# Performance work log

Hardware: AMD Instinct MI355X
Metric: run time of the kernel (lower is better)

Reference implementation:

```python
import jax, jax.numpy as jnp
import numpy as np

N_NODES = 50000
N_EDGES = 800000
NODE_DIM = 128
EDGE_DIM = 10
IN_DIM = 2 * NODE_DIM + EDGE_DIM
BN_EPS = 1e-5


def setup_inputs() -> dict:
    key = jax.random.key(0)
    ks = jax.random.split(key, 8)
    h = jax.random.normal(ks[0], (N_NODES, NODE_DIM), dtype=jnp.float32)
    edge_index = jax.random.randint(ks[1], (2, N_EDGES), 0, N_NODES, dtype=jnp.int64)
    edge_feat = jax.random.normal(ks[2], (N_EDGES, EDGE_DIM), dtype=jnp.float32)
    scale = 1.0 / np.sqrt(IN_DIM)
    gate_w = jax.random.normal(ks[3], (IN_DIM, NODE_DIM), dtype=jnp.float32) * scale
    gate_b = jax.random.normal(ks[4], (NODE_DIM,), dtype=jnp.float32) * scale
    cand_w = jax.random.normal(ks[5], (IN_DIM, NODE_DIM), dtype=jnp.float32) * scale
    cand_b = jax.random.normal(ks[6], (NODE_DIM,), dtype=jnp.float32) * scale
    bn_gamma = jnp.ones((NODE_DIM,), dtype=jnp.float32)
    bn_beta = jnp.zeros((NODE_DIM,), dtype=jnp.float32)
    return {"h": h, "edge_index": edge_index, "edge_feat": edge_feat,
            "gate_w": gate_w, "gate_b": gate_b, "cand_w": cand_w, "cand_b": cand_b,
            "bn_gamma": bn_gamma, "bn_beta": bn_beta}


def reference(h, edge_index, edge_feat, gate_w, gate_b, cand_w, cand_b, bn_gamma, bn_beta):
    src = edge_index[0]
    dst = edge_index[1]
    # gather endpoint features and concat with edge features: [E, 2*D + De]
    z = jnp.concatenate([h[src], h[dst], edge_feat], axis=1)
    g = jax.nn.sigmoid(z @ gate_w + gate_b)   # [E, D]
    c = jax.nn.softplus(z @ cand_w + cand_b)  # [E, D]
    m = g * c
    # scatter-add messages to source nodes (matches index_add_(0, src, m))
    agg = jax.ops.segment_sum(m, src, num_segments=h.shape[0])
    # BatchNorm1d in training mode: batch mean / biased variance over nodes
    mean = jnp.mean(agg, axis=0)
    var = jnp.var(agg, axis=0)
    agg_bn = (agg - mean) * jax.lax.rsqrt(var + BN_EPS) * bn_gamma + bn_beta
    return jax.nn.softplus(h + agg_bn)
```

## Files before the change

### kernel.cpp

```cpp
#include <hip/hip_runtime.h>
#include <math.h>

#define N_NODES 50000
#define N_EDGES 800000
#define D 128
#define DE 10
#define K_TOT 266
#define TE 64
#define N_TILES (N_EDGES / TE)
#define ZSTRIDE 296
#define MSTRIDE 129
#define WP_ELEMS (9 * 16 * 64 * 8)
#define SCAN_BLOCKS 196
#define CSTRIDE 16

typedef __bf16 bf16x8 __attribute__((ext_vector_type(8)));
typedef __bf16 bf16x4 __attribute__((ext_vector_type(4)));
typedef __bf16 bf16x2 __attribute__((ext_vector_type(2)));
typedef float  f32x4  __attribute__((ext_vector_type(4)));

__device__ __forceinline__ float fast_sigmoid(float x) {
    float t = __builtin_amdgcn_exp2f(-1.44269504089f * x);
    return __builtin_amdgcn_rcpf(1.0f + t);
}
__device__ __forceinline__ float fast_softplus(float x) {
    float t = __builtin_amdgcn_exp2f(-1.44269504089f * fabsf(x));
    return fmaxf(x, 0.0f) + 0.69314718056f * __builtin_amdgcn_logf(1.0f + t);
}

__global__ __launch_bounds__(256) void prep(
    const float* __restrict__ h, const float* __restrict__ gw,
    const float* __restrict__ cw, const int* __restrict__ ei,
    __bf16* __restrict__ hb, __bf16* __restrict__ wp,
    int* __restrict__ counts)
{
    int bx = blockIdx.x, t = threadIdx.x;
    if (bx < 6250) {
        int i4 = bx * 256 + t;
        float4 v = *(const float4*)&h[(size_t)i4 * 4];
        bf16x4 o = { (__bf16)v.x, (__bf16)v.y, (__bf16)v.z, (__bf16)v.w };
        *(bf16x4*)&hb[(size_t)i4 * 4] = o;
    } else if (bx < 6538) {
        int idx = (bx - 6250) * 256 + t;
        if (idx < WP_ELEMS) {
            int j    = idx & 7;
            int lane = (idx >> 3) & 63;
            int nb   = (idx >> 9) & 15;
            int kb   = idx >> 13;
            int k    = kb * 32 + ((lane >> 4) << 3) + j;
            int col  = ((nb >> 1) << 4) + (lane & 15);
            const float* w = (nb & 1) ? cw : gw;
            float v = (k < K_TOT) ? w[k * D + col] : 0.0f;
            wp[idx] = (__bf16)v;
        }
    } else {
        int e = (bx - 6538) * 256 + t;
        atomicAdd(&counts[ei[e] * CSTRIDE], 1);
    }
}

__global__ __launch_bounds__(256) void scan_partials(
    const int* __restrict__ counts, int* __restrict__ bsum)
{
    __shared__ int ss[256];
    int t = threadIdx.x;
    int i = blockIdx.x * 256 + t;
    int c = (i < N_NODES) ? counts[i * CSTRIDE] : 0;
    ss[t] = c;
    __syncthreads();
    #pragma unroll
    for (int off = 1; off < 256; off <<= 1) {
        int v = (t >= off) ? ss[t - off] : 0;
        __syncthreads();
        ss[t] += v;
        __syncthreads();
    }
    if (t == 255) bsum[blockIdx.x] = ss[255];
}

__global__ __launch_bounds__(256) void scan_final(
    int* __restrict__ counts, const int* __restrict__ bsum)
{
    __shared__ int sb[256];
    __shared__ int ss[256];
    int t = threadIdx.x;
    sb[t] = (t < SCAN_BLOCKS) ? bsum[t] : 0;
    int i = blockIdx.x * 256 + t;
    int c = (i < N_NODES) ? counts[i * CSTRIDE] : 0;
    ss[t] = c;
    __syncthreads();
    #pragma unroll
    for (int off = 1; off < 256; off <<= 1) {
        int v  = (t >= off) ? ss[t - off] : 0;
        int vb = (t >= off) ? sb[t - off] : 0;
        __syncthreads();
        ss[t] += v;
        sb[t] += vb;
        __syncthreads();
    }
    int base = blockIdx.x ? sb[blockIdx.x - 1] : 0;
    if (i < N_NODES) counts[i * CSTRIDE] = base + ss[t] - c;
}

__global__ __launch_bounds__(256) void csr_scatter(
    const int* __restrict__ ei, int* __restrict__ cursor,
    int2* __restrict__ sdp, int* __restrict__ eidx)
{
    int e = blockIdx.x * 256 + threadIdx.x;
    int node = ei[e];
    int pos = atomicAdd(&cursor[node * CSTRIDE], 1);
    sdp[pos] = make_int2(node, ei[N_EDGES + e]);
    eidx[pos] = e;
}

__global__ __launch_bounds__(256, 4) void edge_mfma_scatter(
    const __bf16* __restrict__ hb, const int2* __restrict__ sdp,
    const float* __restrict__ ef, const __bf16* __restrict__ wp,
    const float* __restrict__ gb, const float* __restrict__ cb,
    const int* __restrict__ eidx, float* __restrict__ agg)
{
    __shared__ __align__(16) unsigned char smem[TE * ZSTRIDE * 2];
    __shared__ int s_eid[TE], s_src[TE], s_dst[TE];
    __bf16* zs = (__bf16*)smem;
    float*  ms = (float*)smem;

    const int t  = threadIdx.x;
    const int e0 = blockIdx.x * TE;

    if (t < TE) {
        int2 p = sdp[e0 + t];
        s_src[t] = p.x;
        s_dst[t] = p.y;
        s_eid[t] = eidx[e0 + t];
    }
    __syncthreads();

    #pragma unroll
    for (int it = 0; it < 8; ++it) {
        int lin = it * 256 + t;
        int region = lin >> 10;
        int r   = (lin >> 4) & 63;
        int seg = lin & 15;
        int node = region ? s_dst[r] : s_src[r];
        bf16x8 v = *(const bf16x8*)&hb[(size_t)node * D + seg * 8];
        *(bf16x8*)&zs[r * ZSTRIDE + region * 128 + seg * 8] = v;
    }
    if (t < TE) {
        const float* efr = &ef[(size_t)s_eid[t] * DE];
        __bf16* row = &zs[t * ZSTRIDE + 256];
        #pragma unroll
        for (int j = 0; j < 5; ++j) {
            float2 a = *(const float2*)&efr[j * 2];
            bf16x2 p = { (__bf16)a.x, (__bf16)a.y };
            *(bf16x2*)&row[j * 2] = p;
        }
        *(bf16x2*)&row[10] = (bf16x2)(__bf16)0.0f;
        *(bf16x4*)&row[12] = (bf16x4)(__bf16)0.0f;
        *(bf16x8*)&row[16] = (bf16x8)(__bf16)0.0f;
        *(bf16x8*)&row[24] = (bf16x8)(__bf16)0.0f;
    }
    __syncthreads();

    const int w     = t >> 6;
    const int l     = t & 63;
    const int quad  = l >> 4;
    const int col16 = l & 15;

    f32x4 acc[4][4];
    #pragma unroll
    for (int mt = 0; mt < 4; ++mt)
        #pragma unroll
        for (int nt = 0; nt < 4; ++nt)
            acc[mt][nt] = (f32x4)0.0f;

    const __bf16* zp  = &zs[col16 * ZSTRIDE + quad * 8];
    const __bf16* wpp = &wp[(size_t)((w * 4) * 64 + l) * 8];

    #pragma unroll
    for (int kb = 0; kb < 9; ++kb) {
        bf16x8 afr[4];
        #pragma unroll
        for (int mt = 0; mt < 4; ++mt)
            afr[mt] = *(const bf16x8*)&zp[mt * 16 * ZSTRIDE + kb * 32];
        bf16x8 bfr[4];
        #pragma unroll
        for (int nt = 0; nt < 4; ++nt)
            bfr[nt] = *(const bf16x8*)&wpp[(size_t)(kb * 16 + nt) * 512];
        #pragma unroll
        for (int mt = 0; mt < 4; ++mt)
            #pragma unroll
            for (int nt = 0; nt < 4; ++nt)
                acc[mt][nt] = __builtin_amdgcn_mfma_f32_16x16x32_bf16(
                    afr[mt], bfr[nt], acc[mt][nt], 0, 0, 0);
    }
    __syncthreads();

    const int colA = w * 32 + col16;
    const int colB = colA + 16;
    const float gbA = gb[colA], cbA = cb[colA];
    const float gbB = gb[colB], cbB = cb[colB];

    #pragma unroll
    for (int mt = 0; mt < 4; ++mt) {
        #pragma unroll
        for (int r = 0; r < 4; ++r) {
            int e = mt * 16 + quad * 4 + r;
            ms[e * MSTRIDE + colA] =
                fast_sigmoid(acc[mt][0][r] + gbA) * fast_softplus(acc[mt][1][r] + cbA);
            ms[e * MSTRIDE + colB] =
                fast_sigmoid(acc[mt][2][r] + gbB) * fast_softplus(acc[mt][3][r] + cbB);
        }
    }
    __syncthreads();

    const int half = t >> 7;
    const int c    = t & 127;
    const int rlo  = half * 32, rhi = rlo + 32;
    int   cur = s_src[rlo];
    float s   = 0.0f;
    for (int e = rlo; e < rhi; ++e) {
        int node = s_src[e];
        float v  = ms[e * MSTRIDE + c];
        if (node != cur) {
            atomicAdd(&agg[(size_t)cur * D + c], s);
            s = 0.0f; cur = node;
        }
        s += v;
    }
    atomicAdd(&agg[(size_t)cur * D + c], s);
}

__global__ __launch_bounds__(256) void col_stats(
    const float* __restrict__ agg, float* __restrict__ stats)
{
    const int t    = threadIdx.x;
    const int col  = t & 127;
    const int half = t >> 7;
    float s = 0.0f, s2 = 0.0f;
    for (int r = blockIdx.x * 2 + half; r < N_NODES; r += gridDim.x * 2) {
        float v = agg[(size_t)r * D + col];
        s += v; s2 += v * v;
    }
    atomicAdd(&stats[col], s);
    atomicAdd(&stats[128 + col], s2);
}

__global__ __launch_bounds__(256) void out_softplus(
    const float* __restrict__ h, const float* __restrict__ agg,
    const float* __restrict__ stats, const float* __restrict__ gamma,
    const float* __restrict__ beta, float* __restrict__ out)
{
    __shared__ float sc[128], bi[128];
    int t = threadIdx.x;
    if (t < 128) {
        const float inv_n = 1.0f / (float)N_NODES;
        float mean = stats[t] * inv_n;
        float var  = stats[128 + t] * inv_n - mean * mean;
        var = fmaxf(var, 0.0f);
        float rstd = rsqrtf(var + 1e-5f);
        float s = rstd * gamma[t];
        sc[t] = s;
        bi[t] = beta[t] - mean * s;
    }
    __syncthreads();
    int idx4 = blockIdx.x * 256 + t;
    int base = idx4 * 4;
    if (base < N_NODES * D) {
        float4 hv = *(const float4*)&h[base];
        float4 av = *(const float4*)&agg[base];
        int c = base & 127;
        float4 o;
        o.x = fast_softplus(hv.x + av.x * sc[c + 0] + bi[c + 0]);
        o.y = fast_softplus(hv.y + av.y * sc[c + 1] + bi[c + 1]);
        o.z = fast_softplus(hv.z + av.z * sc[c + 2] + bi[c + 2]);
        o.w = fast_softplus(hv.w + av.w * sc[c + 3] + bi[c + 3]);
        *(float4*)&out[base] = o;
    }
}

extern "C" void kernel_launch(void* const* d_in, const int* in_sizes, int n_in,
                              void* d_out, int out_size, void* d_ws, size_t ws_size,
                              hipStream_t stream) {
    const float* h     = (const float*)d_in[0];
    const int*   ei    = (const int*)  d_in[1];
    const float* ef    = (const float*)d_in[2];
    const float* gw    = (const float*)d_in[3];
    const float* gb    = (const float*)d_in[4];
    const float* cw    = (const float*)d_in[5];
    const float* cb    = (const float*)d_in[6];
    const float* gamma = (const float*)d_in[7];
    const float* beta  = (const float*)d_in[8];
    float* out = (float*)d_out;

    float*  agg     = (float*)d_ws;
    float*  stats   = agg + (size_t)N_NODES * D;
    int*    counts  = (int*)(stats + 256);
    int*    bsum    = counts + N_NODES * CSTRIDE;
    __bf16* wp      = (__bf16*)(bsum + 256);
    __bf16* hb      = wp + WP_ELEMS;
    int2*   sdp     = (int2*)(hb + (size_t)N_NODES * D);
    int*    eidx    = (int*)(sdp + N_EDGES);

    const size_t zero_bytes = ((size_t)N_NODES * D + 256) * sizeof(float)
                            + (size_t)N_NODES * CSTRIDE * sizeof(int);
    hipMemsetAsync(d_ws, 0, zero_bytes, stream);
    prep<<<9663, 256, 0, stream>>>(h, gw, cw, ei, hb, wp, counts);
    scan_partials<<<SCAN_BLOCKS, 256, 0, stream>>>(counts, bsum);
    scan_final<<<SCAN_BLOCKS, 256, 0, stream>>>(counts, bsum);
    csr_scatter<<<N_EDGES / 256, 256, 0, stream>>>(ei, counts, sdp, eidx);
    edge_mfma_scatter<<<N_TILES, 256, 0, stream>>>(hb, sdp, ef, wp, gb, cb, eidx, agg);
    col_stats<<<784, 256, 0, stream>>>(agg, stats);
    out_softplus<<<(N_NODES * D / 4 + 255) / 256, 256, 0, stream>>>(
        h, agg, stats, gamma, beta, out);
}
```

Baseline: 403.7 us.

## Use 512-thread edge blocks with 16-column MFMA split and packed CSR records

The edge kernel now runs with 512 threads (8 waves), each wave owning 16 output columns instead of 32, which halves the accumulator registers per wave and raises occupancy. The CSR scatter writes one int4 record holding src, dst and edge id instead of separate int2 and int arrays, so the edge kernel does one load per edge. The message-staging stride changes to 132, and the segmented reduction uses 16-edge runs per thread, which may issue more atomics. The tradeoff is more waves per block competing for the shared tile, and a larger metadata record per edge.

```diff
diff --git a/kernel.cpp b/kernel.cpp
--- a/kernel.cpp
+++ b/kernel.cpp
@@ -9,7 +9,7 @@
 #define TE 64
 #define N_TILES (N_EDGES / TE)
 #define ZSTRIDE 296
-#define MSTRIDE 129
+#define MSTRIDE 132
 #define WP_ELEMS (9 * 16 * 64 * 8)
 #define SCAN_BLOCKS 196
 #define CSTRIDE 16
@@ -104,20 +104,19 @@
 
 __global__ __launch_bounds__(256) void csr_scatter(
     const int* __restrict__ ei, int* __restrict__ cursor,
-    int2* __restrict__ sdp, int* __restrict__ eidx)
+    int4* __restrict__ sde)
 {
     int e = blockIdx.x * 256 + threadIdx.x;
     int node = ei[e];
     int pos = atomicAdd(&cursor[node * CSTRIDE], 1);
-    sdp[pos] = make_int2(node, ei[N_EDGES + e]);
-    eidx[pos] = e;
-}
-
-__global__ __launch_bounds__(256, 4) void edge_mfma_scatter(
-    const __bf16* __restrict__ hb, const int2* __restrict__ sdp,
+    sde[pos] = make_int4(node, ei[N_EDGES + e], e, 0);
+}
+
+__global__ __launch_bounds__(512, 6) void edge_mfma_scatter(
+    const __bf16* __restrict__ hb, const int4* __restrict__ sde,
     const float* __restrict__ ef, const __bf16* __restrict__ wp,
     const float* __restrict__ gb, const float* __restrict__ cb,
-    const int* __restrict__ eidx, float* __restrict__ agg)
+    float* __restrict__ agg)
 {
     __shared__ __align__(16) unsigned char smem[TE * ZSTRIDE * 2];
     __shared__ int s_eid[TE], s_src[TE], s_dst[TE];
@@ -128,16 +127,16 @@
     const int e0 = blockIdx.x * TE;
 
     if (t < TE) {
-        int2 p = sdp[e0 + t];
+        int4 p = sde[e0 + t];
         s_src[t] = p.x;
         s_dst[t] = p.y;
-        s_eid[t] = eidx[e0 + t];
-    }
-    __syncthreads();
-
-    #pragma unroll
-    for (int it = 0; it < 8; ++it) {
-        int lin = it * 256 + t;
+        s_eid[t] = p.z;
+    }
+    __syncthreads();
+
+    #pragma unroll
+    for (int it = 0; it < 4; ++it) {
+        int lin = it * 512 + t;
         int region = lin >> 10;
         int r   = (lin >> 4) & 63;
         int seg = lin & 15;
@@ -166,15 +165,15 @@
     const int quad  = l >> 4;
     const int col16 = l & 15;
 
-    f32x4 acc[4][4];
+    f32x4 acc[4][2];
     #pragma unroll
     for (int mt = 0; mt < 4; ++mt)
         #pragma unroll
-        for (int nt = 0; nt < 4; ++nt)
-            acc[mt][nt] = (f32x4)0.0f;
+        for (int f = 0; f < 2; ++f)
+            acc[mt][f] = (f32x4)0.0f;
 
     const __bf16* zp  = &zs[col16 * ZSTRIDE + quad * 8];
-    const __bf16* wpp = &wp[(size_t)((w * 4) * 64 + l) * 8];
+    const __bf16* wpp = &wp[(size_t)((w * 2) * 64 + l) * 8];
 
     #pragma unroll
     for (int kb = 0; kb < 9; ++kb) {
@@ -182,40 +181,41 @@
         #pragma unroll
         for (int mt = 0; mt < 4; ++mt)
             afr[mt] = *(const bf16x8*)&zp[mt * 16 * ZSTRIDE + kb * 32];
-        bf16x8 bfr[4];
-        #pragma unroll
-        for (int nt = 0; nt < 4; ++nt)
-            bfr[nt] = *(const bf16x8*)&wpp[(size_t)(kb * 16 + nt) * 512];
+        bf16x8 bfr[2];
+        #pragma unroll
+        for (int f = 0; f < 2; ++f)
+            bfr[f] = *(const bf16x8*)&wpp[(size_t)(kb * 16 + f) * 512];
         #pragma unroll
         for (int mt = 0; mt < 4; ++mt)
             #pragma unroll
-            for (int nt = 0; nt < 4; ++nt)
-                acc[mt][nt] = __builtin_amdgcn_mfma_f32_16x16x32_bf16(
-                    afr[mt], bfr[nt], acc[mt][nt], 0, 0, 0);
-    }
-    __syncthreads();
-
-    const int colA = w * 32 + col16;
-    const int colB = colA + 16;
-    const float gbA = gb[colA], cbA = cb[colA];
-    const float gbB = gb[colB], cbB = cb[colB];
+            for (int f = 0; f < 2; ++f)
+                acc[mt][f] = __builtin_amdgcn_mfma_f32_16x16x32_bf16(
+                    afr[mt], bfr[f], acc[mt][f], 0, 0, 0);
+    }
+    __syncthreads();
+
+    const int col = w * 16 + col16;
+    const float cbv = cb[col];
+    const float gbn = -1.44269504089f * gb[col];
 
     #pragma unroll
     for (int mt = 0; mt < 4; ++mt) {
         #pragma unroll
         for (int r = 0; r < 4; ++r) {
             int e = mt * 16 + quad * 4 + r;
-            ms[e * MSTRIDE + colA] =
-                fast_sigmoid(acc[mt][0][r] + gbA) * fast_softplus(acc[mt][1][r] + cbA);
-            ms[e * MSTRIDE + colB] =
-                fast_sigmoid(acc[mt][2][r] + gbB) * fast_softplus(acc[mt][3][r] + cbB);
+            float garg = fmaf(-1.44269504089f, acc[mt][0][r], gbn);
+            float sg   = __builtin_amdgcn_rcpf(1.0f + __builtin_amdgcn_exp2f(garg));
+            float x    = acc[mt][1][r] + cbv;
+            float tt   = __builtin_amdgcn_exp2f(-1.44269504089f * fabsf(x));
+            float sp   = fmaxf(x, 0.0f) + 0.69314718056f * __builtin_amdgcn_logf(1.0f + tt);
+            ms[e * MSTRIDE + col] = sg * sp;
         }
     }
     __syncthreads();
 
-    const int half = t >> 7;
-    const int c    = t & 127;
-    const int rlo  = half * 32, rhi = rlo + 32;
+    const int seg = t >> 7;
+    const int c   = t & 127;
+    const int rlo = seg * 16, rhi = rlo + 16;
     int   cur = s_src[rlo];
     float s   = 0.0f;
     for (int e = rlo; e < rhi; ++e) {
@@ -298,8 +298,7 @@
     int*    bsum    = counts + N_NODES * CSTRIDE;
     __bf16* wp      = (__bf16*)(bsum + 256);
     __bf16* hb      = wp + WP_ELEMS;
-    int2*   sdp     = (int2*)(hb + (size_t)N_NODES * D);
-    int*    eidx    = (int*)(sdp + N_EDGES);
+    int4*   sde     = (int4*)(hb + (size_t)N_NODES * D);
 
     const size_t zero_bytes = ((size_t)N_NODES * D + 256) * sizeof(float)
                             + (size_t)N_NODES * CSTRIDE * sizeof(int);
@@ -307,8 +306,8 @@
     prep<<<9663, 256, 0, stream>>>(h, gw, cw, ei, hb, wp, counts);
     scan_partials<<<SCAN_BLOCKS, 256, 0, stream>>>(counts, bsum);
     scan_final<<<SCAN_BLOCKS, 256, 0, stream>>>(counts, bsum);
-    csr_scatter<<<N_EDGES / 256, 256, 0, stream>>>(ei, counts, sdp, eidx);
-    edge_mfma_scatter<<<N_TILES, 256, 0, stream>>>(hb, sdp, ef, wp, gb, cb, eidx, agg);
+    csr_scatter<<<N_EDGES / 256, 256, 0, stream>>>(ei, counts, sde);
+    edge_mfma_scatter<<<N_TILES, 512, 0, stream>>>(hb, sde, ef, wp, gb, cb, agg);
     col_stats<<<784, 256, 0, stream>>>(agg, stats);
     out_softplus<<<(N_NODES * D / 4 + 255) / 256, 256, 0, stream>>>(
         h, agg, stats, gamma, beta, out);
```

Measured after the change: 407.9 us. No clear change (+1.0%).

## Precompute per-node projections and reduce edge GEMM to edge-feature part

Applied to the files above, without the earlier changes.

Splits the concatenated linear layer algebraically: the h[src] and h[dst] contributions to the gate and candidate pre-activations are computed once per node (50k rows) in a new node_gemm kernel, not once per edge (800k rows). The edge kernel then only gathers two precomputed bf16 projection rows per edge, adds them, and runs a tiny K=32 MFMA for the 10 edge features before sigmoid*softplus and the segmented scatter. Source and destination indices are packed into 16-bit halves of one int, and workspace and output buffers are reused for the projection tables. This removes most per-edge FLOPs but adds an extra bf16 rounding of the summed projections, depends on node ids fitting in 16 bits, and relies on aliasing the output and counts buffers.

```diff
diff --git a/kernel.cpp b/kernel.cpp
--- a/kernel.cpp
+++ b/kernel.cpp
@@ -5,12 +5,13 @@
 #define N_EDGES 800000
 #define D 128
 #define DE 10
-#define K_TOT 266
 #define TE 64
 #define N_TILES (N_EDGES / TE)
-#define ZSTRIDE 296
-#define MSTRIDE 129
-#define WP_ELEMS (9 * 16 * 64 * 8)
+#define SST 132
+#define ASTR 136
+#define OST 520
+#define WP2_ELEMS (4 * 32 * 64 * 8)
+#define WEF_ELEMS (16 * 64 * 8)
 #define SCAN_BLOCKS 196
 #define CSTRIDE 16
 
@@ -29,32 +30,37 @@
 }
 
 __global__ __launch_bounds__(256) void prep(
-    const float* __restrict__ h, const float* __restrict__ gw,
-    const float* __restrict__ cw, const int* __restrict__ ei,
-    __bf16* __restrict__ hb, __bf16* __restrict__ wp,
+    const float* __restrict__ gw, const float* __restrict__ cw,
+    const int* __restrict__ ei,
+    __bf16* __restrict__ wp2, __bf16* __restrict__ wef,
     int* __restrict__ counts)
 {
     int bx = blockIdx.x, t = threadIdx.x;
-    if (bx < 6250) {
-        int i4 = bx * 256 + t;
-        float4 v = *(const float4*)&h[(size_t)i4 * 4];
-        bf16x4 o = { (__bf16)v.x, (__bf16)v.y, (__bf16)v.z, (__bf16)v.w };
-        *(bf16x4*)&hb[(size_t)i4 * 4] = o;
-    } else if (bx < 6538) {
-        int idx = (bx - 6250) * 256 + t;
-        if (idx < WP_ELEMS) {
-            int j    = idx & 7;
-            int lane = (idx >> 3) & 63;
-            int nb   = (idx >> 9) & 15;
-            int kb   = idx >> 13;
-            int k    = kb * 32 + ((lane >> 4) << 3) + j;
-            int col  = ((nb >> 1) << 4) + (lane & 15);
-            const float* w = (nb & 1) ? cw : gw;
-            float v = (k < K_TOT) ? w[k * D + col] : 0.0f;
-            wp[idx] = (__bf16)v;
-        }
+    if (bx < 256) {
+        int idx = bx * 256 + t;
+        int j    = idx & 7;
+        int lane = (idx >> 3) & 63;
+        int nb   = (idx >> 9) & 31;
+        int kb   = idx >> 14;
+        int k    = kb * 32 + ((lane >> 4) << 3) + j;
+        int jp   = nb * 16 + (lane & 15);
+        float v;
+        if      (jp < 128) v = gw[k * D + jp];
+        else if (jp < 256) v = cw[k * D + (jp - 128)];
+        else if (jp < 384) v = gw[(128 + k) * D + (jp - 256)];
+        else               v = cw[(128 + k) * D + (jp - 384)];
+        wp2[idx] = (__bf16)v;
+    } else if (bx < 288) {
+        int idx = (bx - 256) * 256 + t;
+        int j    = idx & 7;
+        int lane = (idx >> 3) & 63;
+        int nb   = idx >> 9;
+        int k    = ((lane >> 4) << 3) + j;
+        int col  = (nb >> 1) * 16 + (lane & 15);
+        const float* w = (nb & 1) ? cw : gw;
+        wef[idx] = (__bf16)((k < 10) ? w[(256 + k) * D + col] : 0.0f);
     } else {
-        int e = (bx - 6538) * 256 + t;
+        int e = (bx - 288) * 256 + t;
         atomicAdd(&counts[ei[e] * CSTRIDE], 1);
     }
 }
@@ -104,68 +110,36 @@
 
 __global__ __launch_bounds__(256) void csr_scatter(
     const int* __restrict__ ei, int* __restrict__ cursor,
-    int2* __restrict__ sdp, int* __restrict__ eidx)
+    int2* __restrict__ sde)
 {
     int e = blockIdx.x * 256 + threadIdx.x;
     int node = ei[e];
     int pos = atomicAdd(&cursor[node * CSTRIDE], 1);
-    sdp[pos] = make_int2(node, ei[N_EDGES + e]);
-    eidx[pos] = e;
-}
-
-__global__ __launch_bounds__(256, 4) void edge_mfma_scatter(
-    const __bf16* __restrict__ hb, const int2* __restrict__ sdp,
-    const float* __restrict__ ef, const __bf16* __restrict__ wp,
-    const float* __restrict__ gb, const float* __restrict__ cb,
-    const int* __restrict__ eidx, float* __restrict__ agg)
-{
-    __shared__ __align__(16) unsigned char smem[TE * ZSTRIDE * 2];
-    __shared__ int s_eid[TE], s_src[TE], s_dst[TE];
-    __bf16* zs = (__bf16*)smem;
-    float*  ms = (float*)smem;
-
+    sde[pos] = make_int2(node | (ei[N_EDGES + e] << 16), e);
+}
+
+__global__ __launch_bounds__(512, 4) void node_gemm(
+    const float* __restrict__ h, const __bf16* __restrict__ wp2,
+    __bf16* __restrict__ pa, __bf16* __restrict__ pb)
+{
+    __shared__ __align__(16) __bf16 sm[64 * OST];
+    __bf16* za = sm;
     const int t  = threadIdx.x;
-    const int e0 = blockIdx.x * TE;
-
-    if (t < TE) {
-        int2 p = sdp[e0 + t];
-        s_src[t] = p.x;
-        s_dst[t] = p.y;
-        s_eid[t] = eidx[e0 + t];
-    }
-    __syncthreads();
-
-    #pragma unroll
-    for (int it = 0; it < 8; ++it) {
-        int lin = it * 256 + t;
-        int region = lin >> 10;
-        int r   = (lin >> 4) & 63;
-        int seg = lin & 15;
-        int node = region ? s_dst[r] : s_src[r];
-        bf16x8 v = *(const bf16x8*)&hb[(size_t)node * D + seg * 8];
-        *(bf16x8*)&zs[r * ZSTRIDE + region * 128 + seg * 8] = v;
-    }
-    if (t < TE) {
-        const float* efr = &ef[(size_t)s_eid[t] * DE];
-        __bf16* row = &zs[t * ZSTRIDE + 256];
-        #pragma unroll
-        for (int j = 0; j < 5; ++j) {
-            float2 a = *(const float2*)&efr[j * 2];
-            bf16x2 p = { (__bf16)a.x, (__bf16)a.y };
-            *(bf16x2*)&row[j * 2] = p;
-        }
-        *(bf16x2*)&row[10] = (bf16x2)(__bf16)0.0f;
-        *(bf16x4*)&row[12] = (bf16x4)(__bf16)0.0f;
-        *(bf16x8*)&row[16] = (bf16x8)(__bf16)0.0f;
-        *(bf16x8*)&row[24] = (bf16x8)(__bf16)0.0f;
-    }
-    __syncthreads();
-
-    const int w     = t >> 6;
-    const int l     = t & 63;
-    const int quad  = l >> 4;
-    const int col16 = l & 15;
-
+    const int r0 = blockIdx.x * 64;
+
+    #pragma unroll
+    for (int it = 0; it < 4; ++it) {
+        int ch  = it * 512 + t;
+        int row = ch >> 5, cs = ch & 31;
+        int node = r0 + row;
+        float4 v = (node < N_NODES) ? *(const float4*)&h[(size_t)node * D + cs * 4]
+                                    : make_float4(0.f, 0.f, 0.f, 0.f);
+        bf16x4 o = { (__bf16)v.x, (__bf16)v.y, (__bf16)v.z, (__bf16)v.w };
+        *(bf16x4*)&za[row * ASTR + cs * 4] = o;
+    }
+    __syncthreads();
+
+    const int w = t >> 6, l = t & 63, quad = l >> 4, col16 = l & 15;
     f32x4 acc[4][4];
     #pragma unroll
     for (int mt = 0; mt < 4; ++mt)
@@ -173,19 +147,19 @@
         for (int nt = 0; nt < 4; ++nt)
             acc[mt][nt] = (f32x4)0.0f;
 
-    const __bf16* zp  = &zs[col16 * ZSTRIDE + quad * 8];
-    const __bf16* wpp = &wp[(size_t)((w * 4) * 64 + l) * 8];
-
-    #pragma unroll
-    for (int kb = 0; kb < 9; ++kb) {
+    const __bf16* zp = &za[col16 * ASTR + quad * 8];
+    const __bf16* bp = &wp2[(size_t)((w * 4) * 64 + l) * 8];
+
+    #pragma unroll
+    for (int kb = 0; kb < 4; ++kb) {
         bf16x8 afr[4];
         #pragma unroll
         for (int mt = 0; mt < 4; ++mt)
-            afr[mt] = *(const bf16x8*)&zp[mt * 16 * ZSTRIDE + kb * 32];
+            afr[mt] = *(const bf16x8*)&zp[mt * 16 * ASTR + kb * 32];
         bf16x8 bfr[4];
         #pragma unroll
         for (int nt = 0; nt < 4; ++nt)
-            bfr[nt] = *(const bf16x8*)&wpp[(size_t)(kb * 16 + nt) * 512];
+            bfr[nt] = *(const bf16x8*)&bp[(size_t)(kb * 32 + nt) * 512];
         #pragma unroll
         for (int mt = 0; mt < 4; ++mt)
             #pragma unroll
@@ -195,39 +169,138 @@
     }
     __syncthreads();
 
-    const int colA = w * 32 + col16;
-    const int colB = colA + 16;
-    const float gbA = gb[colA], cbA = cb[colA];
-    const float gbB = gb[colB], cbB = cb[colB];
+    #pragma unroll
+    for (int mt = 0; mt < 4; ++mt)
+        #pragma unroll
+        for (int nt = 0; nt < 4; ++nt)
+            #pragma unroll
+            for (int r = 0; r < 4; ++r) {
+                int row  = mt * 16 + quad * 4 + r;
+                int colj = (w * 4 + nt) * 16 + col16;
+                sm[row * OST + colj] = (__bf16)acc[mt][nt][r];
+            }
+    __syncthreads();
+
+    #pragma unroll
+    for (int it = 0; it < 8; ++it) {
+        int ch  = it * 512 + t;
+        int row = ch >> 6, cc = ch & 63;
+        int node = r0 + row;
+        if (node < N_NODES) {
+            bf16x8 v = *(const bf16x8*)&sm[row * OST + cc * 8];
+            int j0 = cc * 8;
+            if (j0 < 256) *(bf16x8*)&pa[(size_t)node * 256 + j0]         = v;
+            else          *(bf16x8*)&pb[(size_t)node * 256 + (j0 - 256)] = v;
+        }
+    }
+}
+
+__global__ __launch_bounds__(512, 6) void edge_fuse(
+    const __bf16* __restrict__ pa, const __bf16* __restrict__ pb,
+    const int2* __restrict__ sde, const float* __restrict__ ef,
+    const __bf16* __restrict__ wef,
+    const float* __restrict__ gb, const float* __restrict__ cb,
+    float* __restrict__ agg)
+{
+    __shared__ __align__(16) unsigned int sbuf[TE * SST];
+    __shared__ __align__(16) __bf16 zE[TE * 32];
+    __shared__ int s_src[TE], s_dst[TE], s_eid[TE];
+
+    const int t  = threadIdx.x;
+    const int e0 = blockIdx.x * TE;
+    const int w = t >> 6, l = t & 63, quad = l >> 4, col16 = l & 15;
+
+    const __bf16* wpp = &wef[(size_t)((w * 2) * 64 + l) * 8];
+    bf16x8 bfr0 = *(const bf16x8*)&wpp[0];
+    bf16x8 bfr1 = *(const bf16x8*)&wpp[512];
+    const int c = w * 16 + col16;
+    const float gbv = gb[c], cbv = cb[c];
+
+    if (t < TE) {
+        int2 p = sde[e0 + t];
+        s_src[t] = p.x & 0xFFFF;
+        s_dst[t] = (p.x >> 16) & 0xFFFF;
+        s_eid[t] = p.y;
+    }
+    __syncthreads();
+
+    if (t < TE) {
+        const float* efr = &ef[(size_t)s_eid[t] * DE];
+        __bf16* row = &zE[t * 32];
+        #pragma unroll
+        for (int j = 0; j < 5; ++j) {
+            float2 a = *(const float2*)&efr[j * 2];
+            bf16x2 p = { (__bf16)a.x, (__bf16)a.y };
+            *(bf16x2*)&row[j * 2] = p;
+        }
+        *(bf16x2*)&row[10] = (bf16x2)(__bf16)0.0f;
+        *(bf16x4*)&row[12] = (bf16x4)(__bf16)0.0f;
+        *(bf16x8*)&row[16] = (bf16x8)(__bf16)0.0f;
+        *(bf16x8*)&row[24] = (bf16x8)(__bf16)0.0f;
+    }
+
+    #pragma unroll
+    for (int it = 0; it < 2; ++it) {
+        int id  = it * 512 + t;
+        int e   = id >> 4, grp = id & 15;
+        int src = s_src[e], dst = s_dst[e];
+        int c0  = grp * 8;
+        bf16x8 ag = *(const bf16x8*)&pa[(size_t)src * 256 + c0];
+        bf16x8 ac = *(const bf16x8*)&pa[(size_t)src * 256 + 128 + c0];
+        bf16x8 bg = *(const bf16x8*)&pb[(size_t)dst * 256 + c0];
+        bf16x8 bc = *(const bf16x8*)&pb[(size_t)dst * 256 + 128 + c0];
+        unsigned int wds[8];
+        #pragma unroll
+        for (int j = 0; j < 8; ++j) {
+            float gs = (float)ag[j] + (float)bg[j];
+            float cs = (float)ac[j] + (float)bc[j];
+            bf16x2 pr = { (__bf16)gs, (__bf16)cs };
+            wds[j] = __builtin_bit_cast(unsigned int, pr);
+        }
+        *(uint4*)&sbuf[e * SST + c0]     = *(const uint4*)&wds[0];
+        *(uint4*)&sbuf[e * SST + c0 + 4] = *(const uint4*)&wds[4];
+    }
+    __syncthreads();
+
+    f32x4 acc[4][2];
+    #pragma unroll
+    for (int mt = 0; mt < 4; ++mt) {
+        const bf16x8 a = *(const bf16x8*)&zE[(mt * 16 + col16) * 32 + quad * 8];
+        acc[mt][0] = __builtin_amdgcn_mfma_f32_16x16x32_bf16(a, bfr0, (f32x4)0.0f, 0, 0, 0);
+        acc[mt][1] = __builtin_amdgcn_mfma_f32_16x16x32_bf16(a, bfr1, (f32x4)0.0f, 0, 0, 0);
+    }
 
     #pragma unroll
     for (int mt = 0; mt < 4; ++mt) {
         #pragma unroll
         for (int r = 0; r < 4; ++r) {
             int e = mt * 16 + quad * 4 + r;
-            ms[e * MSTRIDE + colA] =
-                fast_sigmoid(acc[mt][0][r] + gbA) * fast_softplus(acc[mt][1][r] + cbA);
-            ms[e * MSTRIDE + colB] =
-                fast_sigmoid(acc[mt][2][r] + gbB) * fast_softplus(acc[mt][3][r] + cbB);
-        }
-    }
-    __syncthreads();
-
-    const int half = t >> 7;
-    const int c    = t & 127;
-    const int rlo  = half * 32, rhi = rlo + 32;
+            unsigned int u = sbuf[e * SST + c];
+            float gs = __builtin_bit_cast(float, u << 16);
+            float cs = __builtin_bit_cast(float, u & 0xFFFF0000u);
+            float sg = fast_sigmoid(acc[mt][0][r] + gs + gbv);
+            float sp = fast_softplus(acc[mt][1][r] + cs + cbv);
+            ((float*)sbuf)[e * SST + c] = sg * sp;
+        }
+    }
+    __syncthreads();
+
+    const int seg = t >> 7;
+    const int cc  = t & 127;
+    const int rlo = seg * 16, rhi = rlo + 16;
     int   cur = s_src[rlo];
     float s   = 0.0f;
+    const float* ms = (const float*)sbuf;
     for (int e = rlo; e < rhi; ++e) {
         int node = s_src[e];
-        float v  = ms[e * MSTRIDE + c];
+        float v  = ms[e * SST + cc];
         if (node != cur) {
-            atomicAdd(&agg[(size_t)cur * D + c], s);
+            atomicAdd(&agg[(size_t)cur * D + cc], s);
             s = 0.0f; cur = node;
         }
         s += v;
     }
-    atomicAdd(&agg[(size_t)cur * D + c], s);
+    atomicAdd(&agg[(size_t)cur * D + cc], s);
 }
 
 __global__ __launch_bounds__(256) void col_stats(
@@ -292,23 +365,26 @@
     const float* beta  = (const float*)d_in[8];
     float* out = (float*)d_out;
 
-    float*  agg     = (float*)d_ws;
-    float*  stats   = agg + (size_t)N_NODES * D;
-    int*    counts  = (int*)(stats + 256);
-    int*    bsum    = counts + N_NODES * CSTRIDE;
-    __bf16* wp      = (__bf16*)(bsum + 256);
-    __bf16* hb      = wp + WP_ELEMS;
-    int2*   sdp     = (int2*)(hb + (size_t)N_NODES * D);
-    int*    eidx    = (int*)(sdp + N_EDGES);
+    float*  agg    = (float*)d_ws;
+    float*  stats  = agg + (size_t)N_NODES * D;
+    int*    counts = (int*)(stats + 256);
+    int*    bsum   = counts + N_NODES * CSTRIDE;
+    __bf16* pb     = (__bf16*)counts;
+    char*   afterU = (char*)counts + (size_t)N_NODES * 256 * sizeof(__bf16);
+    __bf16* wp2    = (__bf16*)afterU;
+    __bf16* wef    = wp2 + WP2_ELEMS;
+    int2*   sde    = (int2*)(wef + WEF_ELEMS);
+    __bf16* pa     = (__bf16*)d_out;
 
     const size_t zero_bytes = ((size_t)N_NODES * D + 256) * sizeof(float)
                             + (size_t)N_NODES * CSTRIDE * sizeof(int);
     hipMemsetAsync(d_ws, 0, zero_bytes, stream);
-    prep<<<9663, 256, 0, stream>>>(h, gw, cw, ei, hb, wp, counts);
+    prep<<<3413, 256, 0, stream>>>(gw, cw, ei, wp2, wef, counts);
     scan_partials<<<SCAN_BLOCKS, 256, 0, stream>>>(counts, bsum);
     scan_final<<<SCAN_BLOCKS, 256, 0, stream>>>(counts, bsum);
-    csr_scatter<<<N_EDGES / 256, 256, 0, stream>>>(ei, counts, sdp, eidx);
-    edge_mfma_scatter<<<N_TILES, 256, 0, stream>>>(hb, sdp, ef, wp, gb, cb, eidx, agg);
+    csr_scatter<<<N_EDGES / 256, 256, 0, stream>>>(ei, counts, sde);
+    node_gemm<<<(N_NODES + 63) / 64, 512, 0, stream>>>(h, wp2, pa, pb);
+    edge_fuse<<<N_TILES, 512, 0, stream>>>(pa, pb, sde, ef, wef, gb, cb, agg);
     col_stats<<<784, 256, 0, stream>>>(agg, stats);
     out_softplus<<<(N_NODES * D / 4 + 255) / 256, 256, 0, stream>>>(
         h, agg, stats, gamma, beta, out);
```

New measurement: 375.8 us. 6.9% less time.
